# Kernel optimization log

Hardware: AMD Instinct MI355X
Metric: run time of the kernel (lower is better)

## Reference

```python
import jax, jax.numpy as jnp
import numpy as np

N_NODES = 100000
N_EDGES = 1600000
NFEAT = 512
HIDDEN = 128
NCLASS = 40


def setup_inputs() -> dict:
    key = jax.random.key(0)
    ks = jax.random.split(key, 8)
    x = jax.random.normal(ks[0], (N_NODES, NFEAT), dtype=jnp.float32)
    edge_src = jax.random.randint(ks[1], (N_EDGES,), 0, N_NODES, dtype=jnp.int32)
    edge_dst = jax.random.randint(ks[2], (N_EDGES,), 0, N_NODES, dtype=jnp.int32)
    # normalized adjacency values (D^-1/2 A D^-1/2 style), all positive
    edge_val = jax.random.uniform(ks[3], (N_EDGES,), dtype=jnp.float32)
    # glorot-ish init like pygcn's reset_parameters
    W1 = jax.random.normal(ks[4], (NFEAT, HIDDEN), dtype=jnp.float32) / np.sqrt(NFEAT)
    b1 = jnp.zeros((HIDDEN,), dtype=jnp.float32)
    W2 = jax.random.normal(ks[5], (HIDDEN, NCLASS), dtype=jnp.float32) / np.sqrt(HIDDEN)
    b2 = jnp.zeros((NCLASS,), dtype=jnp.float32)
    return {"x": x, "edge_src": edge_src, "edge_dst": edge_dst, "edge_val": edge_val,
            "W1": W1, "b1": b1, "W2": W2, "b2": b2}


def _gcn_layer(h, edge_src, edge_dst, edge_val, W, b):
    # support = h @ W ; out = spmm(adj, support) + b
    support = h @ W                                  # [N, d_out]
    msg = support[edge_src] * edge_val[:, None]      # [E, d_out] gather
    agg = jax.ops.segment_sum(msg, edge_dst, num_segments=N_NODES)  # scatter-add
    return agg + b


def reference(x, edge_src, edge_dst, edge_val, W1, b1, W2, b2):
    h = _gcn_layer(x, edge_src, edge_dst, edge_val, W1, b1)
    h = jax.nn.relu(h)
    # dropout=0.0 -> branch skipped (faithful to `if self.dropout:` with falsy value)
    h = _gcn_layer(h, edge_src, edge_dst, edge_val, W2, b2)
    return jax.nn.log_softmax(h, axis=1)
```

## Files before the change

### kernel.cpp

```cpp
#include <hip/hip_runtime.h>
#include <stdint.h>

#define NN 100000
#define NE 1600000
#define NF 512
#define NH 128
#define NC 40

typedef float f32x4 __attribute__((ext_vector_type(4)));
typedef short bf16x8 __attribute__((ext_vector_type(8)));

__device__ __forceinline__ unsigned short f2bf(float f){
    unsigned u = __float_as_uint(f);
    u = u + 0x7FFFu + ((u >> 16) & 1u);
    return (unsigned short)(u >> 16);
}
__device__ __forceinline__ unsigned pk2(float a, float b){
    return (unsigned)f2bf(a) | ((unsigned)f2bf(b) << 16);
}
__device__ __forceinline__ float bf2f(unsigned short s){
    return __uint_as_float(((unsigned)s) << 16);
}
__device__ __forceinline__ float blo(unsigned u){ return __uint_as_float(u << 16); }
__device__ __forceinline__ float bhi(unsigned u){ return __uint_as_float(u & 0xffff0000u); }

__global__ __launch_bounds__(256) void hist_prep(const int* __restrict__ edst,
                       int* __restrict__ deg, int* __restrict__ posw,
                       const float* __restrict__ W1, const float* __restrict__ W2,
                       unsigned short* __restrict__ W1t, unsigned short* __restrict__ W2t){
    if (blockIdx.x < 280){
        int tid = blockIdx.x * 256 + threadIdx.x;
        if (tid < NF * NH){
            int c = tid >> 9;
            int k = tid & 511;
            W1t[c * NF + k] = f2bf(W1[k * NH + c]);
        }
        int t2 = tid - NF * NH;
        if (t2 >= 0 && t2 < 48 * NH){
            int c = t2 >> 7;
            int k = t2 & 127;
            W2t[c * NH + k] = (c < NC) ? f2bf(W2[k * NC + c]) : (unsigned short)0;
        }
    } else {
        int tid = (blockIdx.x - 280) * 256 + threadIdx.x;
        if (tid < NE){
            int d = edst[tid];
            posw[tid] = atomicAdd(&deg[d], 1);
        }
    }
}

__global__ __launch_bounds__(256, 3) void gemm1(const float* __restrict__ x,
                                                const unsigned short* __restrict__ W1t,
                                                unsigned short* __restrict__ s1){
    __shared__ unsigned short Al[128 * 40];
    __shared__ unsigned short Bl[128 * 40];
    const int tid  = threadIdx.x;
    const int wid  = tid >> 6;
    const int lane = tid & 63;
    const int quad = lane >> 4;
    const int l15  = lane & 15;
    const int br   = blockIdx.x * 128;

    const int r    = tid >> 1;
    const int half = tid & 1;

    int arow = br + r; if (arow >= NN) arow = NN - 1;
    const float* aptr = x + (size_t)arow * NF + half * 16;
    const unsigned short* bptr = W1t + (size_t)r * NF + half * 16;

    float4 pa0, pa1, pa2, pa3;
    uint4  pb0, pb1;
    {
        const float4* ap = (const float4*)aptr;
        pa0 = ap[0]; pa1 = ap[1]; pa2 = ap[2]; pa3 = ap[3];
        const uint4* bp = (const uint4*)bptr;
        pb0 = bp[0]; pb1 = bp[1];
    }

    f32x4 acc[2][8];
#pragma unroll
    for (int i = 0; i < 2; i++)
#pragma unroll
        for (int j = 0; j < 8; j++) acc[i][j] = (f32x4){0.f, 0.f, 0.f, 0.f};

    for (int ks = 0; ks < NF; ks += 32){
        unsigned* Ad = (unsigned*)&Al[r * 40 + half * 16];
        Ad[0] = pk2(pa0.x, pa0.y); Ad[1] = pk2(pa0.z, pa0.w);
        Ad[2] = pk2(pa1.x, pa1.y); Ad[3] = pk2(pa1.z, pa1.w);
        Ad[4] = pk2(pa2.x, pa2.y); Ad[5] = pk2(pa2.z, pa2.w);
        Ad[6] = pk2(pa3.x, pa3.y); Ad[7] = pk2(pa3.z, pa3.w);
        uint4* Bd = (uint4*)&Bl[r * 40 + half * 16];
        Bd[0] = pb0; Bd[1] = pb1;
        __syncthreads();

        if (ks + 32 < NF){
            const float4* ap = (const float4*)(aptr + ks + 32);
            pa0 = ap[0]; pa1 = ap[1]; pa2 = ap[2]; pa3 = ap[3];
            const uint4* bp = (const uint4*)(bptr + ks + 32);
            pb0 = bp[0]; pb1 = bp[1];
        }

        bf16x8 a0 = *(const bf16x8*)&Al[(wid * 32 +      l15) * 40 + quad * 8];
        bf16x8 a1 = *(const bf16x8*)&Al[(wid * 32 + 16 + l15) * 40 + quad * 8];
        bf16x8 bb[8];
#pragma unroll
        for (int ct = 0; ct < 8; ct++)
            bb[ct] = *(const bf16x8*)&Bl[(ct * 16 + l15) * 40 + quad * 8];
#pragma unroll
        for (int ct = 0; ct < 8; ct++){
            acc[0][ct] = __builtin_amdgcn_mfma_f32_16x16x32_bf16(a0, bb[ct], acc[0][ct], 0, 0, 0);
            acc[1][ct] = __builtin_amdgcn_mfma_f32_16x16x32_bf16(a1, bb[ct], acc[1][ct], 0, 0, 0);
        }
        __syncthreads();
    }

#pragma unroll
    for (int rt = 0; rt < 2; rt++)
#pragma unroll
        for (int ct = 0; ct < 8; ct++)
#pragma unroll
            for (int i = 0; i < 4; i++){
                int row = br + wid * 32 + rt * 16 + quad * 4 + i;
                if (row < NN) s1[(size_t)row * NH + ct * 16 + l15] = f2bf(acc[rt][ct][i]);
            }
}

__global__ void scan1(const int* __restrict__ deg, int* __restrict__ rs, int* __restrict__ bsums){
    __shared__ int sh[256];
    int t = threadIdx.x;
    int base = blockIdx.x * 1024 + t * 4;
    int v0 = (base     < NN) ? deg[base]     : 0;
    int v1 = (base + 1 < NN) ? deg[base + 1] : 0;
    int v2 = (base + 2 < NN) ? deg[base + 2] : 0;
    int v3 = (base + 3 < NN) ? deg[base + 3] : 0;
    int ssum = v0 + v1 + v2 + v3;
    sh[t] = ssum;
    __syncthreads();
    for (int o = 1; o < 256; o <<= 1){
        int tmp = (t >= o) ? sh[t - o] : 0;
        __syncthreads();
        sh[t] += tmp;
        __syncthreads();
    }
    int excl = sh[t] - ssum;
    if (base     < NN) rs[base]     = excl; excl += v0;
    if (base + 1 < NN) rs[base + 1] = excl; excl += v1;
    if (base + 2 < NN) rs[base + 2] = excl; excl += v2;
    if (base + 3 < NN) rs[base + 3] = excl;
    if (t == 255) bsums[blockIdx.x] = sh[255];
}

__global__ void scan3(int* __restrict__ rs, const int* __restrict__ bsums){
    __shared__ int add_s;
    int t = threadIdx.x;
    if (t < 64){
        int v = 0;
        if (t      < blockIdx.x) v  = bsums[t];
        if (t + 64 < blockIdx.x) v += bsums[t + 64];
#pragma unroll
        for (int o = 32; o; o >>= 1) v += __shfl_xor(v, o, 64);
        if (t == 0) add_s = v;
    }
    __syncthreads();
    int add = add_s;
    int base = blockIdx.x * 1024 + t * 4;
#pragma unroll
    for (int i = 0; i < 4; i++)
        if (base + i < NN) rs[base + i] += add;
}

__global__ __launch_bounds__(256) void scatter_k(const int* __restrict__ esrc, const int* __restrict__ edst,
                          const float* __restrict__ eval, const int* __restrict__ rs,
                          const int* __restrict__ posw, int2* __restrict__ pk){
    int tid = blockIdx.x * 256 + threadIdx.x;
    if (tid < NE){
        int d = edst[tid];
        int pos = rs[d] + posw[tid];
        pk[pos] = make_int2(esrc[tid], __float_as_int(eval[tid]));
    }
}

__global__ __launch_bounds__(256) void agg1(const unsigned* __restrict__ s1v,
                                            const int* __restrict__ rs,
                                            const int2* __restrict__ pk,
                                            const float* __restrict__ b1, unsigned* __restrict__ h){
    int node = blockIdx.x * 4 + (threadIdx.x >> 6);
    if (node >= NN) return;
    int lane = threadIdx.x & 63;
    int s = __builtin_amdgcn_readfirstlane(rs[node]);
    int e = __builtin_amdgcn_readfirstlane((node == NN - 1) ? NE : rs[node + 1]);
    float a0 = 0.f, a1 = 0.f;
    for (int base = s; base < e; base += 64){
        int cnt = e - base; if (cnt > 64) cnt = 64;
        int2 rec = make_int2(0, 0);
        if (base + lane < e) rec = pk[base + lane];
        int j = 0;
        for (; j + 8 <= cnt; j += 8){
            int i0 = __shfl(rec.x, j + 0, 64), i1 = __shfl(rec.x, j + 1, 64);
            int i2 = __shfl(rec.x, j + 2, 64), i3 = __shfl(rec.x, j + 3, 64);
            int i4 = __shfl(rec.x, j + 4, 64), i5 = __shfl(rec.x, j + 5, 64);
            int i6 = __shfl(rec.x, j + 6, 64), i7 = __shfl(rec.x, j + 7, 64);
            unsigned u0 = s1v[(size_t)i0 * 64 + lane];
            unsigned u1 = s1v[(size_t)i1 * 64 + lane];
            unsigned u2 = s1v[(size_t)i2 * 64 + lane];
            unsigned u3 = s1v[(size_t)i3 * 64 + lane];
            unsigned u4 = s1v[(size_t)i4 * 64 + lane];
            unsigned u5 = s1v[(size_t)i5 * 64 + lane];
            unsigned u6 = s1v[(size_t)i6 * 64 + lane];
            unsigned u7 = s1v[(size_t)i7 * 64 + lane];
            float v0 = __int_as_float(__shfl(rec.y, j + 0, 64));
            float v1 = __int_as_float(__shfl(rec.y, j + 1, 64));
            float v2 = __int_as_float(__shfl(rec.y, j + 2, 64));
            float v3 = __int_as_float(__shfl(rec.y, j + 3, 64));
            float v4 = __int_as_float(__shfl(rec.y, j + 4, 64));
            float v5 = __int_as_float(__shfl(rec.y, j + 5, 64));
            float v6 = __int_as_float(__shfl(rec.y, j + 6, 64));
            float v7 = __int_as_float(__shfl(rec.y, j + 7, 64));
            a0 += v0 * blo(u0); a1 += v0 * bhi(u0);
            a0 += v1 * blo(u1); a1 += v1 * bhi(u1);
            a0 += v2 * blo(u2); a1 += v2 * bhi(u2);
            a0 += v3 * blo(u3); a1 += v3 * bhi(u3);
            a0 += v4 * blo(u4); a1 += v4 * bhi(u4);
            a0 += v5 * blo(u5); a1 += v5 * bhi(u5);
            a0 += v6 * blo(u6); a1 += v6 * bhi(u6);
            a0 += v7 * blo(u7); a1 += v7 * bhi(u7);
        }
        for (; j < cnt; j++){
            int   i0 = __shfl(rec.x, j, 64);
            float v0 = __int_as_float(__shfl(rec.y, j, 64));
            unsigned u0 = s1v[(size_t)i0 * 64 + lane];
            a0 += v0 * blo(u0); a1 += v0 * bhi(u0);
        }
    }
    a0 += b1[2 * lane];     a1 += b1[2 * lane + 1];
    a0 = fmaxf(a0, 0.f);    a1 = fmaxf(a1, 0.f);
    h[(size_t)node * 64 + lane] = pk2(a0, a1);
}

__global__ __launch_bounds__(256) void gemm2(const unsigned short* __restrict__ h,
                                             const unsigned short* __restrict__ W2t,
                                             unsigned short* __restrict__ s2p){
    const int tid  = threadIdx.x;
    const int wid  = tid >> 6;
    const int lane = tid & 63;
    const int quad = lane >> 4;
    const int l15  = lane & 15;
    const int row0 = blockIdx.x * 64 + wid * 16;

    bf16x8 bf[3][4];
#pragma unroll
    for (int ct = 0; ct < 3; ct++)
#pragma unroll
        for (int ks = 0; ks < 4; ks++)
            bf[ct][ks] = *(const bf16x8*)&W2t[(ct * 16 + l15) * NH + ks * 32 + quad * 8];

    int arow = row0 + l15; if (arow >= NN) arow = NN - 1;
    const unsigned short* ap = h + (size_t)arow * NH;

    bf16x8 a[4];
#pragma unroll
    for (int ks = 0; ks < 4; ks++) a[ks] = *(const bf16x8*)&ap[ks * 32 + quad * 8];

    f32x4 acc[3];
#pragma unroll
    for (int ct = 0; ct < 3; ct++) acc[ct] = (f32x4){0.f, 0.f, 0.f, 0.f};
#pragma unroll
    for (int ks = 0; ks < 4; ks++)
#pragma unroll
        for (int ct = 0; ct < 3; ct++)
            acc[ct] = __builtin_amdgcn_mfma_f32_16x16x32_bf16(a[ks], bf[ct][ks], acc[ct], 0, 0, 0);

#pragma unroll
    for (int ct = 0; ct < 3; ct++)
#pragma unroll
        for (int i = 0; i < 4; i++){
            int row = row0 + quad * 4 + i;
            if (row < NN) s2p[(size_t)row * 64 + ct * 16 + l15] = f2bf(acc[ct][i]);
        }
}

__global__ __launch_bounds__(256) void agg2(const unsigned short* __restrict__ s2p,
                                            const int* __restrict__ rs,
                                            const int2* __restrict__ pk,
                                            const float* __restrict__ b2, float* __restrict__ out){
    int node = blockIdx.x * 4 + (threadIdx.x >> 6);
    if (node >= NN) return;
    int lane = threadIdx.x & 63;
    int s = __builtin_amdgcn_readfirstlane(rs[node]);
    int e = __builtin_amdgcn_readfirstlane((node == NN - 1) ? NE : rs[node + 1]);
    float a = 0.f;
    for (int base = s; base < e; base += 64){
        int cnt = e - base; if (cnt > 64) cnt = 64;
        int2 rec = make_int2(0, 0);
        if (base + lane < e) rec = pk[base + lane];
        int j = 0;
        for (; j + 8 <= cnt; j += 8){
            int i0 = __shfl(rec.x, j + 0, 64), i1 = __shfl(rec.x, j + 1, 64);
            int i2 = __shfl(rec.x, j + 2, 64), i3 = __shfl(rec.x, j + 3, 64);
            int i4 = __shfl(rec.x, j + 4, 64), i5 = __shfl(rec.x, j + 5, 64);
            int i6 = __shfl(rec.x, j + 6, 64), i7 = __shfl(rec.x, j + 7, 64);
            float g0 = bf2f(s2p[(size_t)i0 * 64 + lane]);
            float g1 = bf2f(s2p[(size_t)i1 * 64 + lane]);
            float g2 = bf2f(s2p[(size_t)i2 * 64 + lane]);
            float g3 = bf2f(s2p[(size_t)i3 * 64 + lane]);
            float g4 = bf2f(s2p[(size_t)i4 * 64 + lane]);
            float g5 = bf2f(s2p[(size_t)i5 * 64 + lane]);
            float g6 = bf2f(s2p[(size_t)i6 * 64 + lane]);
            float g7 = bf2f(s2p[(size_t)i7 * 64 + lane]);
            a += __int_as_float(__shfl(rec.y, j + 0, 64)) * g0;
            a += __int_as_float(__shfl(rec.y, j + 1, 64)) * g1;
            a += __int_as_float(__shfl(rec.y, j + 2, 64)) * g2;
            a += __int_as_float(__shfl(rec.y, j + 3, 64)) * g3;
            a += __int_as_float(__shfl(rec.y, j + 4, 64)) * g4;
            a += __int_as_float(__shfl(rec.y, j + 5, 64)) * g5;
            a += __int_as_float(__shfl(rec.y, j + 6, 64)) * g6;
            a += __int_as_float(__shfl(rec.y, j + 7, 64)) * g7;
        }
        for (; j < cnt; j++){
            int   i0 = __shfl(rec.x, j, 64);
            float v0 = __int_as_float(__shfl(rec.y, j, 64));
            a += v0 * bf2f(s2p[(size_t)i0 * 64 + lane]);
        }
    }
    bool act = lane < NC;
    float z = act ? (a + b2[lane]) : -INFINITY;
    float m = z;
#pragma unroll
    for (int o = 32; o; o >>= 1) m = fmaxf(m, __shfl_xor(m, o, 64));
    float pexp = act ? __expf(z - m) : 0.f;
    float ssum = pexp;
#pragma unroll
    for (int o = 32; o; o >>= 1) ssum += __shfl_xor(ssum, o, 64);
    if (act) out[(size_t)node * NC + lane] = z - m - __logf(ssum);
}

extern "C" void kernel_launch(void* const* d_in, const int* in_sizes, int n_in,
                              void* d_out, int out_size, void* d_ws, size_t ws_size,
                              hipStream_t stream) {
    const float* x    = (const float*)d_in[0];
    const int*   esrc = (const int*)  d_in[1];
    const int*   edst = (const int*)  d_in[2];
    const float* eval = (const float*)d_in[3];
    const float* W1   = (const float*)d_in[4];
    const float* b1   = (const float*)d_in[5];
    const float* W2   = (const float*)d_in[6];
    const float* b2   = (const float*)d_in[7];
    float* out = (float*)d_out;

    char* ws = (char*)d_ws;
    size_t off = 0;
    auto alloc = [&](size_t bytes) -> void* {
        void* p = ws + off;
        off += (bytes + 255) & ~(size_t)255;
        return p;
    };
    unsigned short* W1t  = (unsigned short*)alloc((size_t)NF * NH * 2);
    unsigned short* W2t  = (unsigned short*)alloc((size_t)48 * NH * 2);
    unsigned short* s1   = (unsigned short*)alloc((size_t)NN * NH * 2);
    unsigned short* h    = (unsigned short*)alloc((size_t)NN * NH * 2);
    unsigned short* s2p  = (unsigned short*)alloc((size_t)NN * 64 * 2);
    int*   deg   = (int*)  alloc((size_t)NN * 4);
    int*   rs    = (int*)  alloc((size_t)NN * 4);
    int*   bsums = (int*)  alloc(128 * 4);
    int*   posw  = (int*)  alloc((size_t)NE * 4);
    int2*  pk    = (int2*) alloc((size_t)NE * 8);

    hipMemsetAsync(deg, 0, (size_t)NN * 4, stream);

    hist_prep<<<280 + (NE + 255) / 256, 256, 0, stream>>>(edst, deg, posw, W1, W2, W1t, W2t);
    gemm1    <<<(NN + 127) / 128, 256, 0, stream>>>(x, W1t, s1);
    scan1    <<<98, 256, 0, stream>>>(deg, rs, bsums);
    scan3    <<<98, 256, 0, stream>>>(rs, bsums);
    scatter_k<<<(NE + 255) / 256, 256, 0, stream>>>(esrc, edst, eval, rs, posw, pk);
    agg1     <<<NN / 4, 256, 0, stream>>>((const unsigned*)s1, rs, pk, b1, (unsigned*)h);
    gemm2    <<<(NN + 63) / 64, 256, 0, stream>>>(h, W2t, s2p);
    agg2     <<<NN / 4, 256, 0, stream>>>(s2p, rs, pk, b2, out);
}
```

Baseline: 574.7 us.

## Double-buffer gemm1 LDS tiles and process two nodes per wavefront in aggregation

The gemm1 shared-memory tiles are double-buffered, so the next K-slice is written into the alternate buffer after the MFMAs and each iteration needs one barrier instead of two. Both aggregation kernels now give each half-wavefront its own node, with 32 lanes loading wider vectors (uint2 or packed bf16 pairs). This raises memory-level parallelism for the average degree of about 16 and stops half the lanes idling in agg2, where only 40 of 64 columns were active. The cost is doubled LDS in gemm1, which may limit occupancy, and more divergence between the two half-wave nodes when their degrees differ.

```diff
diff --git a/kernel.cpp b/kernel.cpp
--- a/kernel.cpp
+++ b/kernel.cpp
@@ -53,8 +53,8 @@
 __global__ __launch_bounds__(256, 3) void gemm1(const float* __restrict__ x,
                                                 const unsigned short* __restrict__ W1t,
                                                 unsigned short* __restrict__ s1){
-    __shared__ unsigned short Al[128 * 40];
-    __shared__ unsigned short Bl[128 * 40];
+    __shared__ unsigned short Al[2][128 * 40];
+    __shared__ unsigned short Bl[2][128 * 40];
     const int tid  = threadIdx.x;
     const int wid  = tid >> 6;
     const int lane = tid & 63;
@@ -76,43 +76,56 @@
         pa0 = ap[0]; pa1 = ap[1]; pa2 = ap[2]; pa3 = ap[3];
         const uint4* bp = (const uint4*)bptr;
         pb0 = bp[0]; pb1 = bp[1];
-    }
-
-    f32x4 acc[2][8];
-#pragma unroll
-    for (int i = 0; i < 2; i++)
-#pragma unroll
-        for (int j = 0; j < 8; j++) acc[i][j] = (f32x4){0.f, 0.f, 0.f, 0.f};
-
-    for (int ks = 0; ks < NF; ks += 32){
-        unsigned* Ad = (unsigned*)&Al[r * 40 + half * 16];
+        unsigned* Ad = (unsigned*)&Al[0][r * 40 + half * 16];
         Ad[0] = pk2(pa0.x, pa0.y); Ad[1] = pk2(pa0.z, pa0.w);
         Ad[2] = pk2(pa1.x, pa1.y); Ad[3] = pk2(pa1.z, pa1.w);
         Ad[4] = pk2(pa2.x, pa2.y); Ad[5] = pk2(pa2.z, pa2.w);
         Ad[6] = pk2(pa3.x, pa3.y); Ad[7] = pk2(pa3.z, pa3.w);
-        uint4* Bd = (uint4*)&Bl[r * 40 + half * 16];
+        uint4* Bd = (uint4*)&Bl[0][r * 40 + half * 16];
         Bd[0] = pb0; Bd[1] = pb1;
-        __syncthreads();
-
-        if (ks + 32 < NF){
+    }
+    __syncthreads();
+
+    f32x4 acc[2][8];
+#pragma unroll
+    for (int i = 0; i < 2; i++)
+#pragma unroll
+        for (int j = 0; j < 8; j++) acc[i][j] = (f32x4){0.f, 0.f, 0.f, 0.f};
+
+    int cur = 0;
+    for (int ks = 0; ks < NF; ks += 32){
+        const bool more = (ks + 32 < NF);
+        if (more){
             const float4* ap = (const float4*)(aptr + ks + 32);
             pa0 = ap[0]; pa1 = ap[1]; pa2 = ap[2]; pa3 = ap[3];
             const uint4* bp = (const uint4*)(bptr + ks + 32);
             pb0 = bp[0]; pb1 = bp[1];
         }
 
-        bf16x8 a0 = *(const bf16x8*)&Al[(wid * 32 +      l15) * 40 + quad * 8];
-        bf16x8 a1 = *(const bf16x8*)&Al[(wid * 32 + 16 + l15) * 40 + quad * 8];
+        bf16x8 a0 = *(const bf16x8*)&Al[cur][(wid * 32 +      l15) * 40 + quad * 8];
+        bf16x8 a1 = *(const bf16x8*)&Al[cur][(wid * 32 + 16 + l15) * 40 + quad * 8];
         bf16x8 bb[8];
 #pragma unroll
         for (int ct = 0; ct < 8; ct++)
-            bb[ct] = *(const bf16x8*)&Bl[(ct * 16 + l15) * 40 + quad * 8];
+            bb[ct] = *(const bf16x8*)&Bl[cur][(ct * 16 + l15) * 40 + quad * 8];
 #pragma unroll
         for (int ct = 0; ct < 8; ct++){
             acc[0][ct] = __builtin_amdgcn_mfma_f32_16x16x32_bf16(a0, bb[ct], acc[0][ct], 0, 0, 0);
             acc[1][ct] = __builtin_amdgcn_mfma_f32_16x16x32_bf16(a1, bb[ct], acc[1][ct], 0, 0, 0);
         }
+
+        if (more){
+            int nxt = cur ^ 1;
+            unsigned* Ad = (unsigned*)&Al[nxt][r * 40 + half * 16];
+            Ad[0] = pk2(pa0.x, pa0.y); Ad[1] = pk2(pa0.z, pa0.w);
+            Ad[2] = pk2(pa1.x, pa1.y); Ad[3] = pk2(pa1.z, pa1.w);
+            Ad[4] = pk2(pa2.x, pa2.y); Ad[5] = pk2(pa2.z, pa2.w);
+            Ad[6] = pk2(pa3.x, pa3.y); Ad[7] = pk2(pa3.z, pa3.w);
+            uint4* Bd = (uint4*)&Bl[nxt][r * 40 + half * 16];
+            Bd[0] = pb0; Bd[1] = pb1;
+        }
         __syncthreads();
+        cur ^= 1;
     }
 
 #pragma unroll
@@ -181,61 +194,54 @@
     }
 }
 
-__global__ __launch_bounds__(256) void agg1(const unsigned* __restrict__ s1v,
+__global__ __launch_bounds__(256) void agg1(const uint2* __restrict__ s1v,
                                             const int* __restrict__ rs,
                                             const int2* __restrict__ pk,
-                                            const float* __restrict__ b1, unsigned* __restrict__ h){
-    int node = blockIdx.x * 4 + (threadIdx.x >> 6);
-    if (node >= NN) return;
-    int lane = threadIdx.x & 63;
-    int s = __builtin_amdgcn_readfirstlane(rs[node]);
-    int e = __builtin_amdgcn_readfirstlane((node == NN - 1) ? NE : rs[node + 1]);
-    float a0 = 0.f, a1 = 0.f;
-    for (int base = s; base < e; base += 64){
-        int cnt = e - base; if (cnt > 64) cnt = 64;
+                                            const float* __restrict__ b1, uint2* __restrict__ h){
+    const int lane  = threadIdx.x & 63;
+    const int half  = lane >> 5;
+    const int hl    = lane & 31;
+    const int lbase = half * 32;
+    const int node  = blockIdx.x * 8 + (threadIdx.x >> 6) * 2 + half;
+
+    int s = rs[node];
+    int e = (node == NN - 1) ? NE : rs[node + 1];
+    float a0 = 0.f, a1 = 0.f, a2 = 0.f, a3 = 0.f;
+
+    for (int base = s; base < e; base += 32){
+        int cnt = e - base; if (cnt > 32) cnt = 32;
         int2 rec = make_int2(0, 0);
-        if (base + lane < e) rec = pk[base + lane];
+        if (hl < cnt) rec = pk[base + hl];
         int j = 0;
         for (; j + 8 <= cnt; j += 8){
-            int i0 = __shfl(rec.x, j + 0, 64), i1 = __shfl(rec.x, j + 1, 64);
-            int i2 = __shfl(rec.x, j + 2, 64), i3 = __shfl(rec.x, j + 3, 64);
-            int i4 = __shfl(rec.x, j + 4, 64), i5 = __shfl(rec.x, j + 5, 64);
-            int i6 = __shfl(rec.x, j + 6, 64), i7 = __shfl(rec.x, j + 7, 64);
-            unsigned u0 = s1v[(size_t)i0 * 64 + lane];
-            unsigned u1 = s1v[(size_t)i1 * 64 + lane];
-            unsigned u2 = s1v[(size_t)i2 * 64 + lane];
-            unsigned u3 = s1v[(size_t)i3 * 64 + lane];
-            unsigned u4 = s1v[(size_t)i4 * 64 + lane];
-            unsigned u5 = s1v[(size_t)i5 * 64 + lane];
-            unsigned u6 = s1v[(size_t)i6 * 64 + lane];
-            unsigned u7 = s1v[(size_t)i7 * 64 + lane];
-            float v0 = __int_as_float(__shfl(rec.y, j + 0, 64));
-            float v1 = __int_as_float(__shfl(rec.y, j + 1, 64));
-            float v2 = __int_as_float(__shfl(rec.y, j + 2, 64));
-            float v3 = __int_as_float(__shfl(rec.y, j + 3, 64));
-            float v4 = __int_as_float(__shfl(rec.y, j + 4, 64));
-            float v5 = __int_as_float(__shfl(rec.y, j + 5, 64));
-            float v6 = __int_as_float(__shfl(rec.y, j + 6, 64));
-            float v7 = __int_as_float(__shfl(rec.y, j + 7, 64));
-            a0 += v0 * blo(u0); a1 += v0 * bhi(u0);
-            a0 += v1 * blo(u1); a1 += v1 * bhi(u1);
-            a0 += v2 * blo(u2); a1 += v2 * bhi(u2);
-            a0 += v3 * blo(u3); a1 += v3 * bhi(u3);
-            a0 += v4 * blo(u4); a1 += v4 * bhi(u4);
-            a0 += v5 * blo(u5); a1 += v5 * bhi(u5);
-            a0 += v6 * blo(u6); a1 += v6 * bhi(u6);
-            a0 += v7 * blo(u7); a1 += v7 * bhi(u7);
+            int is[8];
+#pragma unroll
+            for (int q = 0; q < 8; q++) is[q] = __shfl(rec.x, lbase + j + q, 64);
+            uint2 us[8];
+#pragma unroll
+            for (int q = 0; q < 8; q++) us[q] = s1v[(size_t)is[q] * 32 + hl];
+            float vs[8];
+#pragma unroll
+            for (int q = 0; q < 8; q++) vs[q] = __int_as_float(__shfl(rec.y, lbase + j + q, 64));
+#pragma unroll
+            for (int q = 0; q < 8; q++){
+                a0 += vs[q] * blo(us[q].x); a1 += vs[q] * bhi(us[q].x);
+                a2 += vs[q] * blo(us[q].y); a3 += vs[q] * bhi(us[q].y);
+            }
         }
         for (; j < cnt; j++){
-            int   i0 = __shfl(rec.x, j, 64);
-            float v0 = __int_as_float(__shfl(rec.y, j, 64));
-            unsigned u0 = s1v[(size_t)i0 * 64 + lane];
-            a0 += v0 * blo(u0); a1 += v0 * bhi(u0);
-        }
-    }
-    a0 += b1[2 * lane];     a1 += b1[2 * lane + 1];
-    a0 = fmaxf(a0, 0.f);    a1 = fmaxf(a1, 0.f);
-    h[(size_t)node * 64 + lane] = pk2(a0, a1);
+            int   i0 = __shfl(rec.x, lbase + j, 64);
+            float v0 = __int_as_float(__shfl(rec.y, lbase + j, 64));
+            uint2 u  = s1v[(size_t)i0 * 32 + hl];
+            a0 += v0 * blo(u.x); a1 += v0 * bhi(u.x);
+            a2 += v0 * blo(u.y); a3 += v0 * bhi(u.y);
+        }
+    }
+    a0 += b1[4 * hl];     a1 += b1[4 * hl + 1];
+    a2 += b1[4 * hl + 2]; a3 += b1[4 * hl + 3];
+    a0 = fmaxf(a0, 0.f); a1 = fmaxf(a1, 0.f);
+    a2 = fmaxf(a2, 0.f); a3 = fmaxf(a3, 0.f);
+    h[(size_t)node * 32 + hl] = make_uint2(pk2(a0, a1), pk2(a2, a3));
 }
 
 __global__ __launch_bounds__(256) void gemm2(const unsigned short* __restrict__ h,
@@ -280,59 +286,61 @@
         }
 }
 
-__global__ __launch_bounds__(256) void agg2(const unsigned short* __restrict__ s2p,
+__global__ __launch_bounds__(256) void agg2(const unsigned* __restrict__ s2v,
                                             const int* __restrict__ rs,
                                             const int2* __restrict__ pk,
                                             const float* __restrict__ b2, float* __restrict__ out){
-    int node = blockIdx.x * 4 + (threadIdx.x >> 6);
-    if (node >= NN) return;
-    int lane = threadIdx.x & 63;
-    int s = __builtin_amdgcn_readfirstlane(rs[node]);
-    int e = __builtin_amdgcn_readfirstlane((node == NN - 1) ? NE : rs[node + 1]);
-    float a = 0.f;
-    for (int base = s; base < e; base += 64){
-        int cnt = e - base; if (cnt > 64) cnt = 64;
+    const int lane  = threadIdx.x & 63;
+    const int half  = lane >> 5;
+    const int hl    = lane & 31;
+    const int lbase = half * 32;
+    const int node  = blockIdx.x * 8 + (threadIdx.x >> 6) * 2 + half;
+
+    int s = rs[node];
+    int e = (node == NN - 1) ? NE : rs[node + 1];
+    float a0 = 0.f, a1 = 0.f;
+
+    for (int base = s; base < e; base += 32){
+        int cnt = e - base; if (cnt > 32) cnt = 32;
         int2 rec = make_int2(0, 0);
-        if (base + lane < e) rec = pk[base + lane];
+        if (hl < cnt) rec = pk[base + hl];
         int j = 0;
         for (; j + 8 <= cnt; j += 8){
-            int i0 = __shfl(rec.x, j + 0, 64), i1 = __shfl(rec.x, j + 1, 64);
-            int i2 = __shfl(rec.x, j + 2, 64), i3 = __shfl(rec.x, j + 3, 64);
-            int i4 = __shfl(rec.x, j + 4, 64), i5 = __shfl(rec.x, j + 5, 64);
-            int i6 = __shfl(rec.x, j + 6, 64), i7 = __shfl(rec.x, j + 7, 64);
-            float g0 = bf2f(s2p[(size_t)i0 * 64 + lane]);
-            float g1 = bf2f(s2p[(size_t)i1 * 64 + lane]);
-            float g2 = bf2f(s2p[(size_t)i2 * 64 + lane]);
-            float g3 = bf2f(s2p[(size_t)i3 * 64 + lane]);
-            float g4 = bf2f(s2p[(size_t)i4 * 64 + lane]);
-            float g5 = bf2f(s2p[(size_t)i5 * 64 + lane]);
-            float g6 = bf2f(s2p[(size_t)i6 * 64 + lane]);
-            float g7 = bf2f(s2p[(size_t)i7 * 64 + lane]);
-            a += __int_as_float(__shfl(rec.y, j + 0, 64)) * g0;
-            a += __int_as_float(__shfl(rec.y, j + 1, 64)) * g1;
-            a += __int_as_float(__shfl(rec.y, j + 2, 64)) * g2;
-            a += __int_as_float(__shfl(rec.y, j + 3, 64)) * g3;
-            a += __int_as_float(__shfl(rec.y, j + 4, 64)) * g4;
-            a += __int_as_float(__shfl(rec.y, j + 5, 64)) * g5;
-            a += __int_as_float(__shfl(rec.y, j + 6, 64)) * g6;
-            a += __int_as_float(__shfl(rec.y, j + 7, 64)) * g7;
+            int is[8];
+#pragma unroll
+            for (int q = 0; q < 8; q++) is[q] = __shfl(rec.x, lbase + j + q, 64);
+            unsigned us[8];
+#pragma unroll
+            for (int q = 0; q < 8; q++) us[q] = s2v[(size_t)is[q] * 32 + hl];
+            float vs[8];
+#pragma unroll
+            for (int q = 0; q < 8; q++) vs[q] = __int_as_float(__shfl(rec.y, lbase + j + q, 64));
+#pragma unroll
+            for (int q = 0; q < 8; q++){
+                a0 += vs[q] * blo(us[q]); a1 += vs[q] * bhi(us[q]);
+            }
         }
         for (; j < cnt; j++){
-            int   i0 = __shfl(rec.x, j, 64);
-            float v0 = __int_as_float(__shfl(rec.y, j, 64));
-            a += v0 * bf2f(s2p[(size_t)i0 * 64 + lane]);
-        }
-    }
-    bool act = lane < NC;
-    float z = act ? (a + b2[lane]) : -INFINITY;
-    float m = z;
-#pragma unroll
-    for (int o = 32; o; o >>= 1) m = fmaxf(m, __shfl_xor(m, o, 64));
-    float pexp = act ? __expf(z - m) : 0.f;
-    float ssum = pexp;
-#pragma unroll
-    for (int o = 32; o; o >>= 1) ssum += __shfl_xor(ssum, o, 64);
-    if (act) out[(size_t)node * NC + lane] = z - m - __logf(ssum);
+            int   i0 = __shfl(rec.x, lbase + j, 64);
+            float v0 = __int_as_float(__shfl(rec.y, lbase + j, 64));
+            unsigned u = s2v[(size_t)i0 * 32 + hl];
+            a0 += v0 * blo(u); a1 += v0 * bhi(u);
+        }
+    }
+    bool act = hl < 20;
+    float z0 = act ? (a0 + b2[2 * hl])     : -INFINITY;
+    float z1 = act ? (a1 + b2[2 * hl + 1]) : -INFINITY;
+    float m = fmaxf(z0, z1);
+#pragma unroll
+    for (int o = 16; o; o >>= 1) m = fmaxf(m, __shfl_xor(m, o, 64));
+    float pe = act ? (__expf(z0 - m) + __expf(z1 - m)) : 0.f;
+#pragma unroll
+    for (int o = 16; o; o >>= 1) pe += __shfl_xor(pe, o, 64);
+    if (act){
+        float l = __logf(pe);
+        float2 o2 = make_float2(z0 - m - l, z1 - m - l);
+        *(float2*)(out + (size_t)node * NC + 2 * hl) = o2;
+    }
 }
 
 extern "C" void kernel_launch(void* const* d_in, const int* in_sizes, int n_in,
@@ -373,7 +381,7 @@
     scan1    <<<98, 256, 0, stream>>>(deg, rs, bsums);
     scan3    <<<98, 256, 0, stream>>>(rs, bsums);
     scatter_k<<<(NE + 255) / 256, 256, 0, stream>>>(esrc, edst, eval, rs, posw, pk);
-    agg1     <<<NN / 4, 256, 0, stream>>>((const unsigned*)s1, rs, pk, b1, (unsigned*)h);
+    agg1     <<<NN / 8, 256, 0, stream>>>((const uint2*)s1, rs, pk, b1, (uint2*)h);
     gemm2    <<<(NN + 63) / 64, 256, 0, stream>>>(h, W2t, s2p);
-    agg2     <<<NN / 4, 256, 0, stream>>>(s2p, rs, pk, b2, out);
-}
+    agg2     <<<NN / 8, 256, 0, stream>>>((const unsigned*)s2p, rs, pk, b2, out);
+}
```

Result: faster. 553.5 us (-3.7%).
